# Kernel optimization log

Hardware: AMD Instinct MI355X
Metric: run time of the kernel (lower is better)

The kernel has to match this reference:

```python
import jax, jax.numpy as jnp
from jax import lax
import numpy as np


def setup_inputs() -> dict:
    key = jax.random.key(0)
    k1, k2, k3, k4, k5 = jax.random.split(key, 5)
    bs, m, v, L, P = 2, 16, 16, 40320, 32
    preds = jax.random.normal(k1, (bs, m, v, L), dtype=jnp.float32)
    target = jax.random.normal(k2, (bs, v, L), dtype=jnp.float32)
    weights = jax.random.uniform(k3, (L,), dtype=jnp.float32)
    scale = jax.random.uniform(k4, (v,), dtype=jnp.float32)
    # binary-ish patch masks over grid points (float, as in the torch buffer)
    masks = (jax.random.uniform(k5, (P, L)) < 0.25).astype(jnp.float32)
    return {"preds": preds, "target": target, "weights": weights,
            "scale": scale, "masks": masks, "beta": 1}


def _energy_score(x, y, m, beta):
    # x: (bs, m, D) ensemble, y: (bs, D) observation
    diff = x - y[:, None, :]
    a = jnp.sqrt(jnp.sum(diff * diff, axis=-1))            # (bs, m)
    score_a = jnp.mean(jnp.sum(a ** beta, axis=-1)) / m
    # pairwise distances via Gram trick (cdist p=2)
    sq = jnp.sum(x * x, axis=-1)                            # (bs, m)
    g = jnp.einsum('bid,bjd->bij', x, x)                    # (bs, m, m)
    d2 = jnp.maximum(sq[:, :, None] + sq[:, None, :] - 2.0 * g, 0.0)
    pos = d2 > 0
    d = jnp.where(pos, jnp.sqrt(jnp.where(pos, d2, 1.0)), 0.0)
    score_b = jnp.mean(jnp.sum(d ** beta, axis=(1, 2))) / (2 * m * (m - 1))
    return score_a - score_b


def reference(preds, target, weights, scale, masks, beta):
    beta = float(beta)
    bs, m, v, L = preds.shape
    # buffer scaling as in forward()
    p = preds * scale[None, None, :, None] * weights        # (bs, m, v, L)
    t = target * scale[None, :, None] * weights             # (bs, v, L)

    def body(acc, mask):
        # rearrange 'bs m v latlon -> bs m (latlon v)'
        x = (p * mask).transpose(0, 1, 3, 2).reshape(bs, m, L * v)
        y = (t * mask).transpose(0, 2, 1).reshape(bs, L * v)
        return acc + _energy_score(x, y, m, beta), None

    total, _ = lax.scan(body, jnp.float32(0.0), masks)
    return total
```

## Files before the change

### kernel.cpp

```cpp
#include <hip/hip_runtime.h>
#include <math.h>

#define BS 2
#define M 16
#define V 16
#define NROWB 136
#define NROWS 272
#define PMASK 32
#define NPB 630
#define NE 8704
#define PBSTRIDE 8704
#define SPLIT 30
#define QPB 21

typedef __attribute__((ext_vector_type(8))) short bf16x8;
typedef __attribute__((ext_vector_type(4))) float f32x4;
typedef __attribute__((ext_vector_type(4))) unsigned int u32x4;

#define VMW(n) asm volatile("s_waitcnt vmcnt(" #n ")" ::: "memory")
#define LGKM0  asm volatile("s_waitcnt lgkmcnt(0)" ::: "memory")

static __device__ __forceinline__ unsigned short f2bf(float x) {
    unsigned int u = __float_as_uint(x);
    unsigned int r = (u + 0x7FFFu + ((u >> 16) & 1u)) >> 16;
    return (unsigned short)r;
}

static __device__ __forceinline__ void k1_issue(
    const float* __restrict__ preds, f32x4* __restrict__ r,
    int b, int v0, int l0, int L, int lane, int wave)
{
#pragma unroll
    for (int n = 0; n < 2; ++n) {
        int r0 = wave * 8 + n * 4;
        int rr = r0 + (lane >> 4);
        int grow = b * 256 + (rr >> 1) * 16 + v0 + (rr & 1);
        r[n] = *(const f32x4*)(preds + (size_t)grow * L + l0 + (lane & 15) * 4);
    }
}

static __device__ __forceinline__ void k1_write(
    float* __restrict__ dst, const f32x4* __restrict__ r, int lane, int wave)
{
#pragma unroll
    for (int n = 0; n < 2; ++n) {
        int r0 = wave * 8 + n * 4;
        *(f32x4*)(dst + r0 * 64 + lane * 4) = r[n];
    }
}

template<int W>
static __device__ __forceinline__ void k1_chunk(
    const float* __restrict__ xsb,
    const float* __restrict__ targ,
    const float* __restrict__ scl,
    float wl,
    int v0, int lane, float* __restrict__ acc)
{
    const int base = (W == 0) ? 0 : 34 * W - 16;
    const int npair = (W == 0) ? 18 : 34;
    const int aoff = (W == 0) ? 16 : 0;

#pragma unroll
    for (int vc = 0; vc < 2; ++vc) {
        const int v = v0 + vc;
        float s = scl[v] * wl;
        float x[M];
#pragma unroll
        for (int i = 0; i < M; ++i)
            x[i] = xsb[(i * 2 + vc) * 64 + lane] * s;
        if (W == 0) {
            float y = targ[v] * s;
#pragma unroll
            for (int i = 0; i < M; ++i) {
                float d = x[i] - y;
                acc[i] = fmaf(d, d, acc[i]);
            }
        }
        int k = 0;
#pragma unroll
        for (int i = 0; i < M; ++i) {
#pragma unroll
            for (int j = i + 1; j < M; ++j) {
                if (k >= base && k < base + npair) {
                    float d = x[i] - x[j];
                    acc[aoff + k - base] = fmaf(d, d, acc[aoff + k - base]);
                }
                ++k;
            }
        }
    }
}

__global__ __launch_bounds__(256, 2)
void k1_fused(const float* __restrict__ preds, const float* __restrict__ target,
              const float* __restrict__ weights, const float* __restrict__ scale,
              const float* __restrict__ masks, float* __restrict__ partial,
              float* __restrict__ out, int L)
{
    __shared__ float xs[2][2048];
    __shared__ unsigned short sld[144 * 64];

    const int t = (int)threadIdx.x;
    const int lane = t & 63, wave = t >> 6;
    const int pb = (int)blockIdx.x;
    const int b  = (int)blockIdx.y;
    const int l0 = pb * 64;

    if (pb == 0 && b == 0 && t == 0) out[0] = 0.0f;

    const size_t Ls = (size_t)L;

    const float wl = weights[l0 + lane];
    float scl[V];
#pragma unroll
    for (int v = 0; v < V; ++v) scl[v] = scale[v];
    float targ[V];
    if (wave == 0) {
#pragma unroll
        for (int v = 0; v < V; ++v)
            targ[v] = target[(size_t)(b * V + v) * Ls + l0 + lane];
    }
    VMW(0);
    __builtin_amdgcn_sched_barrier(0);

    f32x4 rb[3][2];
    k1_issue(preds, rb[0], b, 0, l0, L, lane, wave);
    k1_issue(preds, rb[1], b, 2, l0, L, lane, wave);
    k1_issue(preds, rb[2], b, 4, l0, L, lane, wave);
    __builtin_amdgcn_sched_barrier(0);
    VMW(4);
    k1_write(&xs[0][0], rb[0], lane, wave);
    LGKM0;
    __builtin_amdgcn_s_barrier();
    __builtin_amdgcn_sched_barrier(0);

    float acc[34];
#pragma unroll
    for (int r = 0; r < 34; ++r) acc[r] = 0.0f;

#pragma unroll
    for (int s = 0; s < 8; ++s) {
        if (s + 3 < 8) {
            k1_issue(preds, rb[(s + 3) % 3], b, (s + 3) * 2, l0, L, lane, wave);
            __builtin_amdgcn_sched_barrier(0);
        }
        const float* xsb = &xs[s & 1][0];
        switch (wave) {
            case 0: k1_chunk<0>(xsb, targ, scl, wl, s * 2, lane, acc); break;
            case 1: k1_chunk<1>(xsb, targ, scl, wl, s * 2, lane, acc); break;
            case 2: k1_chunk<2>(xsb, targ, scl, wl, s * 2, lane, acc); break;
            default: k1_chunk<3>(xsb, targ, scl, wl, s * 2, lane, acc); break;
        }
        if (s + 1 < 8) {
            if (s < 5)       { VMW(4); }
            else if (s == 5) { VMW(2); }
            else             { VMW(0); }
            k1_write(&xs[(s + 1) & 1][0], rb[(s + 1) % 3], lane, wave);
        }
        LGKM0;
        __builtin_amdgcn_s_barrier();
        __builtin_amdgcn_sched_barrier(0);
    }

    ((unsigned int*)sld)[136 * 32 + t] = 0;

#pragma unroll
    for (int r = 0; r < 34; ++r) {
        const int R = 34 * wave + r;
        sld[R * 64 + (lane ^ ((R & 7) << 3))] = f2bf(acc[r]);
    }
    __syncthreads();

    const int ntile = (wave == 3) ? 3 : 2;
    f32x4 pacc[3][2];
#pragma unroll
    for (int ti = 0; ti < 3; ++ti)
#pragma unroll
        for (int pt = 0; pt < 2; ++pt)
            pacc[ti][pt] = (f32x4){0.f, 0.f, 0.f, 0.f};

#pragma unroll
    for (int ks = 0; ks < 2; ++ks) {
        bf16x8 bfr[2];
#pragma unroll
        for (int pt = 0; pt < 2; ++pt) {
            const float* mp = masks + (size_t)(pt * 16 + (lane & 15)) * Ls
                            + l0 + ks * 32 + (lane >> 4) * 8;
            u32x4 m0 = *(const u32x4*)mp;
            u32x4 m1 = *(const u32x4*)(mp + 4);
            union { unsigned int u[4]; bf16x8 v; } bb;
            bb.u[0] = __builtin_amdgcn_perm(m0.y, m0.x, 0x07060302);
            bb.u[1] = __builtin_amdgcn_perm(m0.w, m0.z, 0x07060302);
            bb.u[2] = __builtin_amdgcn_perm(m1.y, m1.x, 0x07060302);
            bb.u[3] = __builtin_amdgcn_perm(m1.w, m1.z, 0x07060302);
            bfr[pt] = bb.v;
        }
#pragma unroll
        for (int ti = 0; ti < 3; ++ti) {
            if (ti >= ntile) continue;
            const int tile = (ti == 2) ? 8 : (wave + ti * 4);
            const bf16x8 a = *(const bf16x8*)&sld[
                (tile * 16 + (lane & 15)) * 64 +
                ((ks * 32 + (lane >> 4) * 8) ^ ((lane & 7) << 3))];
            pacc[ti][0] = __builtin_amdgcn_mfma_f32_16x16x32_bf16(
                a, bfr[0], pacc[ti][0], 0, 0, 0);
            pacc[ti][1] = __builtin_amdgcn_mfma_f32_16x16x32_bf16(
                a, bfr[1], pacc[ti][1], 0, 0, 0);
        }
    }

    float* P = partial + (size_t)(pb * 2 + b) * (NROWB * PMASK);
#pragma unroll
    for (int ti = 0; ti < 3; ++ti) {
        if (ti >= ntile) continue;
        const int tile = (ti == 2) ? 8 : (wave + ti * 4);
#pragma unroll
        for (int pt = 0; pt < 2; ++pt)
#pragma unroll
            for (int reg = 0; reg < 4; ++reg) {
                const int row = tile * 16 + (lane >> 4) * 4 + reg;
                if (row < NROWB)
                    P[row * 32 + pt * 16 + (lane & 15)] = pacc[ti][pt][reg];
            }
    }
}

__global__ __launch_bounds__(256, 2)
void k3a_reduce(const float* __restrict__ P, float* __restrict__ P2)
{
    const int t = (int)threadIdx.x;
    const int e = (int)blockIdx.x * 256 + t;
    const int spl = (int)blockIdx.y;

    const float* p = P + (size_t)(spl * QPB) * PBSTRIDE + e;
    float a0 = 0.f, a1 = 0.f, a2 = 0.f;
#pragma unroll
    for (int q = 0; q < QPB; q += 3) {
        a0 += p[(size_t)(q    ) * PBSTRIDE];
        a1 += p[(size_t)(q + 1) * PBSTRIDE];
        a2 += p[(size_t)(q + 2) * PBSTRIDE];
    }
    P2[(size_t)spl * NE + e] = (a0 + a1) + a2;
}

__global__ __launch_bounds__(256, 2)
void k3b_finalize(const float* __restrict__ P2, const int* __restrict__ beta_p,
                  float* __restrict__ out)
{
    const int t = (int)threadIdx.x;
    const int e = (int)blockIdx.x * 256 + t;

    float a0 = 0.f, a1 = 0.f, a2 = 0.f;
#pragma unroll
    for (int q = 0; q < SPLIT; q += 3) {
        a0 += P2[(size_t)(q    ) * NE + e];
        a1 += P2[(size_t)(q + 1) * NE + e];
        a2 += P2[(size_t)(q + 2) * NE + e];
    }
    float d2 = fmaxf((a0 + a1) + a2, 0.0f);
    float beta = (float)beta_p[0];
    float d = (beta == 1.0f) ? sqrtf(d2) : powf(d2, 0.5f * beta);

    const float wa = 1.0f / (float)(BS * M);
    const float wb = -1.0f / (float)(BS * M * (M - 1));
    const int row_g = e >> 5;
    const int local = row_g % NROWB;
    float sum = ((local < M) ? wa : wb) * d;

    const int lane = t & 63, wv = t >> 6;
#pragma unroll
    for (int off = 32; off > 0; off >>= 1)
        sum += __shfl_down(sum, off, 64);
    __shared__ float red[4];
    if (lane == 0) red[wv] = sum;
    __syncthreads();
    if (t == 0)
        atomicAdd(out, red[0] + red[1] + red[2] + red[3]);
}

extern "C" void kernel_launch(void* const* d_in, const int* in_sizes, int n_in,
                              void* d_out, int out_size, void* d_ws, size_t ws_size,
                              hipStream_t stream)
{
    const float* preds   = (const float*)d_in[0];
    const float* target  = (const float*)d_in[1];
    const float* weights = (const float*)d_in[2];
    const float* scale   = (const float*)d_in[3];
    const float* masks   = (const float*)d_in[4];
    const int*   beta    = (const int*)d_in[5];
    float* out = (float*)d_out;

    int L = in_sizes[2];

    float* partial = (float*)d_ws;
    size_t p_bytes = (size_t)NPB * 2 * NROWB * PMASK * sizeof(float);
    float* partial2 = (float*)((char*)d_ws + ((p_bytes + 255) & ~(size_t)255));

    dim3 g1(NPB, BS);
    k1_fused<<<g1, 256, 0, stream>>>(preds, target, weights, scale, masks,
                                     partial, out, L);

    dim3 g3a(NE / 256, SPLIT);
    k3a_reduce<<<g3a, 256, 0, stream>>>(partial, partial2);

    k3b_finalize<<<NE / 256, 256, 0, stream>>>(partial2, beta, out);
}
```

Measured before the change: 153.6 us.

## Split variable dimension across two blocks and load all slices upfront

The fused kernel grid gains a third dimension that splits the 16 variables into two halves of 8, doubling the number of blocks and halving each block's serial work. Each block now issues all four preds loads at once into four LDS buffers, replacing the rotating three-deep register pipeline, and reuses the same LDS for the bf16 staging area. Partial results go to twice as many slots, so the downstream reduction reads double the partial data, which adds memory traffic and reduction work in exchange for more parallelism and a shorter per-block critical path.

```diff
diff --git a/kernel.cpp b/kernel.cpp
--- a/kernel.cpp
+++ b/kernel.cpp
@@ -10,8 +10,9 @@
 #define NPB 630
 #define NE 8704
 #define PBSTRIDE 8704
+#define NSLOT 1260
 #define SPLIT 30
-#define QPB 21
+#define QPB 42
 
 typedef __attribute__((ext_vector_type(8))) short bf16x8;
 typedef __attribute__((ext_vector_type(4))) float f32x4;
@@ -28,13 +29,13 @@
 
 static __device__ __forceinline__ void k1_issue(
     const float* __restrict__ preds, f32x4* __restrict__ r,
-    int b, int v0, int l0, int L, int lane, int wave)
+    int b, int v0abs, int l0, int L, int lane, int wave)
 {
 #pragma unroll
     for (int n = 0; n < 2; ++n) {
         int r0 = wave * 8 + n * 4;
         int rr = r0 + (lane >> 4);
-        int grow = b * 256 + (rr >> 1) * 16 + v0 + (rr & 1);
+        int grow = b * 256 + (rr >> 1) * 16 + v0abs + (rr & 1);
         r[n] = *(const f32x4*)(preds + (size_t)grow * L + l0 + (lane & 15) * 4);
     }
 }
@@ -54,8 +55,7 @@
     const float* __restrict__ xsb,
     const float* __restrict__ targ,
     const float* __restrict__ scl,
-    float wl,
-    int v0, int lane, float* __restrict__ acc)
+    float wl, int v0, int lane, float* __restrict__ acc)
 {
     const int base = (W == 0) ? 0 : 34 * W - 16;
     const int npair = (W == 0) ? 18 : 34;
@@ -98,69 +98,61 @@
               const float* __restrict__ masks, float* __restrict__ partial,
               float* __restrict__ out, int L)
 {
-    __shared__ float xs[2][2048];
-    __shared__ unsigned short sld[144 * 64];
+    __shared__ float xs[4][2048];
+    unsigned short* sld = (unsigned short*)&xs[0][0];
 
     const int t = (int)threadIdx.x;
     const int lane = t & 63, wave = t >> 6;
     const int pb = (int)blockIdx.x;
     const int b  = (int)blockIdx.y;
+    const int h  = (int)blockIdx.z;
     const int l0 = pb * 64;
-
-    if (pb == 0 && b == 0 && t == 0) out[0] = 0.0f;
+    const int vbase = h * 8;
+
+    if (pb == 0 && b == 0 && h == 0 && t == 0) out[0] = 0.0f;
 
     const size_t Ls = (size_t)L;
 
     const float wl = weights[l0 + lane];
-    float scl[V];
-#pragma unroll
-    for (int v = 0; v < V; ++v) scl[v] = scale[v];
-    float targ[V];
+    float scl[8];
+#pragma unroll
+    for (int v = 0; v < 8; ++v) scl[v] = scale[vbase + v];
+    float targ[8];
     if (wave == 0) {
 #pragma unroll
-        for (int v = 0; v < V; ++v)
-            targ[v] = target[(size_t)(b * V + v) * Ls + l0 + lane];
+        for (int v = 0; v < 8; ++v)
+            targ[v] = target[(size_t)(b * V + vbase + v) * Ls + l0 + lane];
     }
     VMW(0);
     __builtin_amdgcn_sched_barrier(0);
 
-    f32x4 rb[3][2];
-    k1_issue(preds, rb[0], b, 0, l0, L, lane, wave);
-    k1_issue(preds, rb[1], b, 2, l0, L, lane, wave);
-    k1_issue(preds, rb[2], b, 4, l0, L, lane, wave);
+    f32x4 rb[4][2];
+#pragma unroll
+    for (int s = 0; s < 4; ++s)
+        k1_issue(preds, rb[s], b, vbase + s * 2, l0, L, lane, wave);
     __builtin_amdgcn_sched_barrier(0);
-    VMW(4);
-    k1_write(&xs[0][0], rb[0], lane, wave);
-    LGKM0;
-    __builtin_amdgcn_s_barrier();
-    __builtin_amdgcn_sched_barrier(0);
 
     float acc[34];
 #pragma unroll
     for (int r = 0; r < 34; ++r) acc[r] = 0.0f;
 
 #pragma unroll
-    for (int s = 0; s < 8; ++s) {
-        if (s + 3 < 8) {
-            k1_issue(preds, rb[(s + 3) % 3], b, (s + 3) * 2, l0, L, lane, wave);
-            __builtin_amdgcn_sched_barrier(0);
-        }
-        const float* xsb = &xs[s & 1][0];
+    for (int s = 0; s < 4; ++s) {
+        switch (s) {
+            case 0: VMW(6); break;  case 1: VMW(4); break;
+            case 2: VMW(2); break;  default: VMW(0); break;
+        }
+        k1_write(&xs[s][0], rb[s], lane, wave);
+        LGKM0;
+        __builtin_amdgcn_s_barrier();
+        __builtin_amdgcn_sched_barrier(0);
+        const float* xsb = &xs[s][0];
         switch (wave) {
             case 0: k1_chunk<0>(xsb, targ, scl, wl, s * 2, lane, acc); break;
             case 1: k1_chunk<1>(xsb, targ, scl, wl, s * 2, lane, acc); break;
             case 2: k1_chunk<2>(xsb, targ, scl, wl, s * 2, lane, acc); break;
             default: k1_chunk<3>(xsb, targ, scl, wl, s * 2, lane, acc); break;
         }
-        if (s + 1 < 8) {
-            if (s < 5)       { VMW(4); }
-            else if (s == 5) { VMW(2); }
-            else             { VMW(0); }
-            k1_write(&xs[(s + 1) & 1][0], rb[(s + 1) % 3], lane, wave);
-        }
-        LGKM0;
-        __builtin_amdgcn_s_barrier();
-        __builtin_amdgcn_sched_barrier(0);
     }
 
     ((unsigned int*)sld)[136 * 32 + t] = 0;
@@ -210,7 +202,8 @@
         }
     }
 
-    float* P = partial + (size_t)(pb * 2 + b) * (NROWB * PMASK);
+    float* P = partial + (size_t)(pb * 2 + h) * PBSTRIDE
+             + (size_t)b * (NROWB * PMASK);
 #pragma unroll
     for (int ti = 0; ti < 3; ++ti) {
         if (ti >= ntile) continue;
@@ -294,10 +287,10 @@
     int L = in_sizes[2];
 
     float* partial = (float*)d_ws;
-    size_t p_bytes = (size_t)NPB * 2 * NROWB * PMASK * sizeof(float);
+    size_t p_bytes = (size_t)NSLOT * PBSTRIDE * sizeof(float);
     float* partial2 = (float*)((char*)d_ws + ((p_bytes + 255) & ~(size_t)255));
 
-    dim3 g1(NPB, BS);
+    dim3 g1(NPB, BS, 2);
     k1_fused<<<g1, 256, 0, stream>>>(preds, target, weights, scale, masks,
                                      partial, out, L);
 
```

Result: slower. 157.1 us (+2.3%).
